# Optimization experiments

Measured on AMD Instinct MI355X. Metric: run time of the kernel, lower is better.

The kernel has to match this reference:

```python
import jax, jax.numpy as jnp
import numpy as np

T, B, I, H, L = 512, 64, 512, 1024, 2

def setup_inputs() -> dict:
    key = jax.random.key(0)
    ks = jax.random.split(key, 9)
    stdv = 1.0 / np.sqrt(H)
    u = lambda k, shape: jax.random.uniform(k, shape, jnp.float32, -stdv, stdv)
    return {
        "x": jax.random.normal(ks[0], (T, B, I), jnp.float32),
        "w_ih0": u(ks[1], (4 * H, I)),
        "w_hh0": u(ks[2], (4 * H, H)),
        "b_ih0": u(ks[3], (4 * H,)),
        "b_hh0": u(ks[4], (4 * H,)),
        "w_ih1": u(ks[5], (4 * H, H)),
        "w_hh1": u(ks[6], (4 * H, H)),
        "b_ih1": u(ks[7], (4 * H,)),
        "b_hh1": u(ks[8], (4 * H,)),
    }

def _lstm_cell(x, h, c, w_ih, w_hh, b_ih, b_hh):
    # gates: [B, 4H]
    gates = x @ w_ih.T + b_ih + h @ w_hh.T + b_hh
    i, f, g, o = jnp.split(gates, 4, axis=1)
    c_new = jax.nn.sigmoid(f) * c + jax.nn.sigmoid(i) * jnp.tanh(g)
    h_new = jax.nn.sigmoid(o) * jnp.tanh(c_new)
    return h_new, c_new

def reference(x, w_ih0, w_hh0, b_ih0, b_hh0, w_ih1, w_hh1, b_ih1, b_hh1):
    layers = [(w_ih0, w_hh0, b_ih0, b_hh0), (w_ih1, w_hh1, b_ih1, b_hh1)]
    h0 = jnp.zeros((L, B, H), x.dtype)
    c0 = jnp.zeros((L, B, H), x.dtype)

    def step(carry, x_t):
        h, c = carry
        inp = x_t
        hs, cs = [], []
        for l, (w_ih, w_hh, b_ih, b_hh) in enumerate(layers):
            h_new, c_new = _lstm_cell(inp, h[l], c[l], w_ih, w_hh, b_ih, b_hh)
            hs.append(h_new)
            cs.append(c_new)
            inp = h_new
        return (jnp.stack(hs), jnp.stack(cs)), inp

    (h_f, c_f), out = jax.lax.scan(step, (h0, c0), x)
    return out, (h_f, c_f)
```

## Files before the change

### kernel.cpp

```cpp
#include <hip/hip_runtime.h>

#define TT 512
#define BB 64
#define II 512
#define HH 1024
#define NBLK 256
#define NTHR 512
#define NCTR 32
#define CSTRIDE 32

typedef short bf16x8 __attribute__((ext_vector_type(8)));
typedef float f32x4 __attribute__((ext_vector_type(4)));
typedef int   i32x4 __attribute__((ext_vector_type(4)));

struct Params {
  const unsigned short* xb;
  unsigned short* h0;
  unsigned short* h1;
  unsigned int* ctr;
  const float* wih0; const float* whh0; const float* bih0; const float* bhh0;
  const float* wih1; const float* whh1; const float* bih1; const float* bhh1;
  float* out;
};

__device__ __forceinline__ unsigned short f2bf(float f) {
  unsigned int u = __float_as_uint(f);
  u += 0x7fffu + ((u >> 16) & 1u);
  return (unsigned short)(u >> 16);
}

__device__ __forceinline__ bf16x8 ld_bypass(const unsigned short* p) {
  i32x4 r;
  asm volatile("global_load_dwordx4 %0, %1, off sc0 sc1" : "=v"(r) : "v"(p));
  return __builtin_bit_cast(bf16x8, r);
}

__device__ __forceinline__ void st_bypass_u16(unsigned short* p, unsigned int v) {
  asm volatile("global_store_short %0, %1, off sc0 sc1" :: "v"(p), "v"(v) : "memory");
}

__global__ void cvt_kernel(const float* __restrict__ x, unsigned short* __restrict__ xb, int n8) {
  int i = blockIdx.x * blockDim.x + threadIdx.x;
  int stride = gridDim.x * blockDim.x;
  for (; i < n8; i += stride) {
    const float4* p = (const float4*)(x) + (size_t)i * 2;
    float4 a = p[0], b = p[1];
    bf16x8 v;
    v[0] = (short)f2bf(a.x); v[1] = (short)f2bf(a.y); v[2] = (short)f2bf(a.z); v[3] = (short)f2bf(a.w);
    v[4] = (short)f2bf(b.x); v[5] = (short)f2bf(b.y); v[6] = (short)f2bf(b.z); v[7] = (short)f2bf(b.w);
    ((bf16x8*)xb)[i] = v;
  }
}

__device__ __forceinline__ void gridbar(unsigned int* ctr, unsigned int target, int tid) {
  asm volatile("s_waitcnt vmcnt(0)" ::: "memory");
  __syncthreads();
  if (tid == 0)
    __hip_atomic_fetch_add(&ctr[(blockIdx.x & (NCTR - 1)) * CSTRIDE], 1u,
                           __ATOMIC_RELAXED, __HIP_MEMORY_SCOPE_AGENT);
  if (tid < NCTR) {
    while (__hip_atomic_load(&ctr[tid * CSTRIDE], __ATOMIC_RELAXED,
                             __HIP_MEMORY_SCOPE_AGENT) < target) {
      __builtin_amdgcn_s_sleep(1);
    }
  }
  __syncthreads();
}

template <int LAYER>
__device__ void body(const Params& P, float (*pbuf)[64][36], float (*cb)[16]) {
  constexpr int K   = (LAYER == 0) ? (II + HH) : (2 * HH);
  constexpr int KSL = K / (8 * 32);
  constexpr int KB  = KSL / 2;
  constexpr int KIH = (LAYER == 0) ? II : HH;

  const int tid  = threadIdx.x;
  const int lane = tid & 63;
  const int kh   = tid >> 6;
  const int lbid = blockIdx.x & 127;
  const int mh   = lbid >> 6;
  const int ns   = lbid & 63;
  const int l15  = lane & 15;
  const int lk8  = (lane >> 4) * 8;

  const float* wih = (LAYER == 0) ? P.wih0 : P.wih1;
  const float* whh = (LAYER == 0) ? P.whh0 : P.whh1;

  bf16x8 wf[4][KSL];
  #pragma unroll
  for (int nt = 0; nt < 4; ++nt) {
    const int row = nt * HH + ns * 16 + l15;
    #pragma unroll
    for (int ks = 0; ks < KSL; ++ks) {
      int k = kh * (KSL * 32) + ks * 32 + lk8;
      const float* src = (k < KIH) ? (wih + (size_t)row * KIH + k)
                                   : (whh + (size_t)row * HH + (k - KIH));
      const float4* p4 = (const float4*)src;
      float4 a = p4[0], b = p4[1];
      bf16x8 v;
      v[0] = (short)f2bf(a.x); v[1] = (short)f2bf(a.y); v[2] = (short)f2bf(a.z); v[3] = (short)f2bf(a.w);
      v[4] = (short)f2bf(b.x); v[5] = (short)f2bf(b.y); v[6] = (short)f2bf(b.z); v[7] = (short)f2bf(b.w);
      wf[nt][ks] = v;
    }
  }

  float bv[4];
  {
    const float* bi = (LAYER == 0) ? P.bih0 : P.bih1;
    const float* bh = (LAYER == 0) ? P.bhh0 : P.bhh1;
    int unit = ns * 16 + (tid & 15);
    #pragma unroll
    for (int g = 0; g < 4; ++g) bv[g] = bi[g * HH + unit] + bh[g * HH + unit];
  }

  if (tid < 128) {
    int q = tid >> 4, j = tid & 15;
    #pragma unroll
    for (int r = 0; r < 4; ++r) cb[q * 4 + r][j] = 0.f;
  }

  const size_t BH  = (size_t)BB * HH;
  const size_t TBH = (size_t)TT * BH;

  #pragma unroll 1
  for (int p = 0; p <= TT; ++p) {
    const int t = (LAYER == 0) ? p : p - 1;
    const bool active = (LAYER == 0) ? (p < TT) : (p >= 1);

    f32x4 acc[2][4];
    if (active) {
      #pragma unroll
      for (int mt = 0; mt < 2; ++mt)
        #pragma unroll
        for (int nt = 0; nt < 4; ++nt) acc[mt][nt] = f32x4{0.f, 0.f, 0.f, 0.f};

      const unsigned short* h0prev = P.h0 + (size_t)((t + 1) & 1) * BH;
      const unsigned short* h0cur  = P.h0 + (size_t)(t & 1) * BH;
      const unsigned short* h1prev = P.h1 + (size_t)((t + 1) & 1) * BH;

      #pragma unroll
      for (int half = 0; half < 2; ++half) {
        bf16x8 af[KB][2];
        #pragma unroll
        for (int ksb = 0; ksb < KB; ++ksb) {
          const int ks = half * KB + ksb;
          const int k  = kh * (KSL * 32) + ks * 32 + lk8;
          #pragma unroll
          for (int mt = 0; mt < 2; ++mt) {
            const int m = mh * 32 + mt * 16 + l15;
            if (LAYER == 0) {
              if (k < II) af[ksb][mt] = *(const bf16x8*)(P.xb + ((size_t)t * BB + m) * II + k);
              else        af[ksb][mt] = ld_bypass(h0prev + (size_t)m * HH + (k - II));
            } else {
              if (k < HH) af[ksb][mt] = ld_bypass(h0cur + (size_t)m * HH + k);
              else        af[ksb][mt] = ld_bypass(h1prev + (size_t)m * HH + (k - HH));
            }
          }
        }
        asm volatile("s_waitcnt vmcnt(0)" ::: "memory");
        __builtin_amdgcn_sched_barrier(0);
        #pragma unroll
        for (int ksb = 0; ksb < KB; ++ksb) {
          const int ks = half * KB + ksb;
          #pragma unroll
          for (int mt = 0; mt < 2; ++mt)
            #pragma unroll
            for (int nt = 0; nt < 4; ++nt)
              acc[mt][nt] = __builtin_amdgcn_mfma_f32_16x16x32_bf16(af[ksb][mt], wf[nt][ks], acc[mt][nt], 0, 0, 0);
        }
      }

      if (kh >= 4) {
        #pragma unroll
        for (int mt = 0; mt < 2; ++mt)
          #pragma unroll
          for (int nt = 0; nt < 4; ++nt) {
            int col = nt * 16 + l15;
            int mb  = mt * 16 + (lane >> 4) * 4;
            *(f32x4*)&pbuf[kh - 4][col][mb] = acc[mt][nt];
          }
      }
    }
    __syncthreads();
    if (active && kh < 4) {
      #pragma unroll
      for (int mt = 0; mt < 2; ++mt)
        #pragma unroll
        for (int nt = 0; nt < 4; ++nt) {
          int col = nt * 16 + l15;
          int mb  = mt * 16 + (lane >> 4) * 4;
          f32x4 v = *(const f32x4*)&pbuf[kh][col][mb];
          acc[mt][nt] += v;
          *(f32x4*)&pbuf[kh][col][mb] = acc[mt][nt];
        }
    }
    __syncthreads();
    if (active && tid < 128) {
      int q = tid >> 4, j = tid & 15;
      f32x4 gv[4];
      #pragma unroll
      for (int g = 0; g < 4; ++g) {
        int col = g * 16 + j;
        f32x4 s = *(const f32x4*)&pbuf[0][col][q * 4];
        #pragma unroll
        for (int w = 1; w < 4; ++w) s += *(const f32x4*)&pbuf[w][col][q * 4];
        gv[g] = s;
      }
      #pragma unroll
      for (int r = 0; r < 4; ++r) {
        int m = q * 4 + r;
        float iv = 1.f / (1.f + __expf(-(gv[0][r] + bv[0])));
        float fv = 1.f / (1.f + __expf(-(gv[1][r] + bv[1])));
        float gg = tanhf(gv[2][r] + bv[2]);
        float ov = 1.f / (1.f + __expf(-(gv[3][r] + bv[3])));
        float c = fv * cb[m][j] + iv * gg;
        cb[m][j] = c;
        float h = ov * tanhf(c);
        int mg = mh * 32 + m;
        int unit = ns * 16 + j;
        unsigned int hb = f2bf(h);
        if (LAYER == 0) {
          st_bypass_u16(P.h0 + (size_t)(t & 1) * BH + (size_t)mg * HH + unit, hb);
          if (t == TT - 1) P.out[TBH + (size_t)mg * HH + unit] = h;
        } else {
          st_bypass_u16(P.h1 + (size_t)(t & 1) * BH + (size_t)mg * HH + unit, hb);
          P.out[(size_t)t * BH + (size_t)mg * HH + unit] = h;
          if (t == TT - 1) P.out[TBH + BH + (size_t)mg * HH + unit] = h;
        }
      }
    }
    gridbar(P.ctr, (unsigned)(NBLK / NCTR) * (unsigned)(p + 1), tid);
  }

  if (tid < 128) {
    int q = tid >> 4, j = tid & 15;
    #pragma unroll
    for (int r = 0; r < 4; ++r) {
      int m = q * 4 + r;
      int mg = mh * 32 + m;
      int unit = ns * 16 + j;
      P.out[TBH + (size_t)(2 + LAYER) * BH + (size_t)mg * HH + unit] = cb[m][j];
    }
  }
}

__global__ void __launch_bounds__(NTHR, 2) lstm_kernel(Params P) {
  __shared__ float pbuf[4][64][36];
  __shared__ float cb[32][16];
  if (blockIdx.x < 128) body<0>(P, pbuf, cb);
  else                  body<1>(P, pbuf, cb);
}

extern "C" void kernel_launch(void* const* d_in, const int* in_sizes, int n_in,
                              void* d_out, int out_size, void* d_ws, size_t ws_size,
                              hipStream_t stream) {
  const float* x = (const float*)d_in[0];
  Params P;
  P.wih0 = (const float*)d_in[1];
  P.whh0 = (const float*)d_in[2];
  P.bih0 = (const float*)d_in[3];
  P.bhh0 = (const float*)d_in[4];
  P.wih1 = (const float*)d_in[5];
  P.whh1 = (const float*)d_in[6];
  P.bih1 = (const float*)d_in[7];
  P.bhh1 = (const float*)d_in[8];
  P.out  = (float*)d_out;

  char* ws = (char*)d_ws;
  P.ctr = (unsigned int*)ws;
  P.xb  = (const unsigned short*)(ws + 8192);
  unsigned short* xb_w = (unsigned short*)(ws + 8192);
  P.h0  = (unsigned short*)(ws + 8192 + (size_t)TT * BB * II * 2);
  P.h1  = P.h0 + (size_t)2 * BB * HH;

  hipMemsetAsync((void*)P.ctr, 0, 8192, stream);
  hipMemsetAsync((void*)P.h0, 0, (size_t)4 * BB * HH * sizeof(unsigned short), stream);

  int n8 = TT * BB * II / 8;
  cvt_kernel<<<2048, 256, 0, stream>>>(x, xb_w, n8);

  void* args[] = { &P };
  hipLaunchCooperativeKernel((void*)lstm_kernel, dim3(NBLK), dim3(NTHR), args, 0, stream);
}
```

Baseline: 4.356 ms.

## Stage h in LDS for vector stores, early barrier arrive, pipelined A-loads

Hidden-state outputs are first staged in shared memory, then written with 128-bit cache-bypassing stores instead of scattered 16-bit stores. The grid barrier is split so a block signals arrival right after its h stores, and the fp32 output writes happen before it waits. The A-fragment loads become a double-buffered pipeline in groups of two k-slices with partial vmcnt waits, and the launch-bounds occupancy hint drops from 2 to 1 block per CU, which frees registers. This targets per-step latency on the critical path of the recurrent chain, at the cost of an extra __syncthreads and added register pressure.

```diff
diff --git a/kernel.cpp b/kernel.cpp
--- a/kernel.cpp
+++ b/kernel.cpp
@@ -35,8 +35,8 @@
   return __builtin_bit_cast(bf16x8, r);
 }
 
-__device__ __forceinline__ void st_bypass_u16(unsigned short* p, unsigned int v) {
-  asm volatile("global_store_short %0, %1, off sc0 sc1" :: "v"(p), "v"(v) : "memory");
+__device__ __forceinline__ void st_bypass_b128(unsigned short* p, i32x4 v) {
+  asm volatile("global_store_dwordx4 %0, %1, off sc0 sc1" :: "v"(p), "v"(v) : "memory");
 }
 
 __global__ void cvt_kernel(const float* __restrict__ x, unsigned short* __restrict__ xb, int n8) {
@@ -52,26 +52,12 @@
   }
 }
 
-__device__ __forceinline__ void gridbar(unsigned int* ctr, unsigned int target, int tid) {
-  asm volatile("s_waitcnt vmcnt(0)" ::: "memory");
-  __syncthreads();
-  if (tid == 0)
-    __hip_atomic_fetch_add(&ctr[(blockIdx.x & (NCTR - 1)) * CSTRIDE], 1u,
-                           __ATOMIC_RELAXED, __HIP_MEMORY_SCOPE_AGENT);
-  if (tid < NCTR) {
-    while (__hip_atomic_load(&ctr[tid * CSTRIDE], __ATOMIC_RELAXED,
-                             __HIP_MEMORY_SCOPE_AGENT) < target) {
-      __builtin_amdgcn_s_sleep(1);
-    }
-  }
-  __syncthreads();
-}
-
 template <int LAYER>
-__device__ void body(const Params& P, float (*pbuf)[64][36], float (*cb)[16]) {
+__device__ void body(const Params& P, float (*pbuf)[64][36], float (*cb)[16],
+                     unsigned short (*hbuf)[16]) {
   constexpr int K   = (LAYER == 0) ? (II + HH) : (2 * HH);
   constexpr int KSL = K / (8 * 32);
-  constexpr int KB  = KSL / 2;
+  constexpr int NG  = KSL / 2;
   constexpr int KIH = (LAYER == 0) ? II : HH;
 
   const int tid  = threadIdx.x;
@@ -128,6 +114,7 @@
     const bool active = (LAYER == 0) ? (p < TT) : (p >= 1);
 
     f32x4 acc[2][4];
+    float hv[4];
     if (active) {
       #pragma unroll
       for (int mt = 0; mt < 2; ++mt)
@@ -138,36 +125,46 @@
       const unsigned short* h0cur  = P.h0 + (size_t)(t & 1) * BH;
       const unsigned short* h1prev = P.h1 + (size_t)((t + 1) & 1) * BH;
 
-      #pragma unroll
-      for (int half = 0; half < 2; ++half) {
-        bf16x8 af[KB][2];
-        #pragma unroll
-        for (int ksb = 0; ksb < KB; ++ksb) {
-          const int ks = half * KB + ksb;
+      bf16x8 af[2][2][2];
+
+      auto issue_group = [&](int g, int pp) {
+        #pragma unroll
+        for (int ksb = 0; ksb < 2; ++ksb) {
+          const int ks = g * 2 + ksb;
           const int k  = kh * (KSL * 32) + ks * 32 + lk8;
           #pragma unroll
           for (int mt = 0; mt < 2; ++mt) {
             const int m = mh * 32 + mt * 16 + l15;
+            const unsigned short* src;
             if (LAYER == 0) {
-              if (k < II) af[ksb][mt] = *(const bf16x8*)(P.xb + ((size_t)t * BB + m) * II + k);
-              else        af[ksb][mt] = ld_bypass(h0prev + (size_t)m * HH + (k - II));
+              src = (k < II) ? (P.xb + ((size_t)t * BB + m) * II + k)
+                             : (h0prev + (size_t)m * HH + (k - II));
             } else {
-              if (k < HH) af[ksb][mt] = ld_bypass(h0cur + (size_t)m * HH + k);
-              else        af[ksb][mt] = ld_bypass(h1prev + (size_t)m * HH + (k - HH));
+              src = (k < HH) ? (h0cur + (size_t)m * HH + k)
+                             : (h1prev + (size_t)m * HH + (k - HH));
             }
+            af[pp][ksb][mt] = ld_bypass(src);
           }
         }
-        asm volatile("s_waitcnt vmcnt(0)" ::: "memory");
+      };
+
+      issue_group(0, 0);
+      issue_group(1, 1);
+      #pragma unroll
+      for (int g = 0; g < NG; ++g) {
+        if (g < NG - 1) asm volatile("s_waitcnt vmcnt(4)" ::: "memory");
+        else            asm volatile("s_waitcnt vmcnt(0)" ::: "memory");
         __builtin_amdgcn_sched_barrier(0);
         #pragma unroll
-        for (int ksb = 0; ksb < KB; ++ksb) {
-          const int ks = half * KB + ksb;
+        for (int ksb = 0; ksb < 2; ++ksb) {
+          const int ks = g * 2 + ksb;
           #pragma unroll
           for (int mt = 0; mt < 2; ++mt)
             #pragma unroll
             for (int nt = 0; nt < 4; ++nt)
-              acc[mt][nt] = __builtin_amdgcn_mfma_f32_16x16x32_bf16(af[ksb][mt], wf[nt][ks], acc[mt][nt], 0, 0, 0);
+              acc[mt][nt] = __builtin_amdgcn_mfma_f32_16x16x32_bf16(af[g & 1][ksb][mt], wf[nt][ks], acc[mt][nt], 0, 0, 0);
         }
+        if (g + 2 < NG) issue_group(g + 2, g & 1);
       }
 
       if (kh >= 4) {
@@ -216,20 +213,47 @@
         float c = fv * cb[m][j] + iv * gg;
         cb[m][j] = c;
         float h = ov * tanhf(c);
-        int mg = mh * 32 + m;
+        hv[r] = h;
+        hbuf[m][j] = f2bf(h);
+      }
+    }
+    __syncthreads();
+    if (tid < 64) {
+      if (active) {
+        int row  = tid >> 1;
+        int half = tid & 1;
+        i32x4 v = *(const i32x4*)&hbuf[row][half * 8];
+        unsigned short* dst = ((LAYER == 0) ? P.h0 : P.h1) +
+            (size_t)(t & 1) * BH + (size_t)(mh * 32 + row) * HH + ns * 16 + half * 8;
+        st_bypass_b128(dst, v);
+      }
+      asm volatile("s_waitcnt vmcnt(0)" ::: "memory");
+      if (tid == 0)
+        __hip_atomic_fetch_add(&P.ctr[(blockIdx.x & (NCTR - 1)) * CSTRIDE], 1u,
+                               __ATOMIC_RELAXED, __HIP_MEMORY_SCOPE_AGENT);
+    }
+    if (active && tid < 128) {
+      int q = tid >> 4, j = tid & 15;
+      #pragma unroll
+      for (int r = 0; r < 4; ++r) {
+        int mg = mh * 32 + q * 4 + r;
         int unit = ns * 16 + j;
-        unsigned int hb = f2bf(h);
         if (LAYER == 0) {
-          st_bypass_u16(P.h0 + (size_t)(t & 1) * BH + (size_t)mg * HH + unit, hb);
-          if (t == TT - 1) P.out[TBH + (size_t)mg * HH + unit] = h;
+          if (t == TT - 1) P.out[TBH + (size_t)mg * HH + unit] = hv[r];
         } else {
-          st_bypass_u16(P.h1 + (size_t)(t & 1) * BH + (size_t)mg * HH + unit, hb);
-          P.out[(size_t)t * BH + (size_t)mg * HH + unit] = h;
-          if (t == TT - 1) P.out[TBH + BH + (size_t)mg * HH + unit] = h;
+          P.out[(size_t)t * BH + (size_t)mg * HH + unit] = hv[r];
+          if (t == TT - 1) P.out[TBH + BH + (size_t)mg * HH + unit] = hv[r];
         }
       }
     }
-    gridbar(P.ctr, (unsigned)(NBLK / NCTR) * (unsigned)(p + 1), tid);
+    if (tid < NCTR) {
+      unsigned int target = (unsigned)(NBLK / NCTR) * (unsigned)(p + 1);
+      while (__hip_atomic_load(&P.ctr[tid * CSTRIDE], __ATOMIC_RELAXED,
+                               __HIP_MEMORY_SCOPE_AGENT) < target) {
+        __builtin_amdgcn_s_sleep(1);
+      }
+    }
+    __syncthreads();
   }
 
   if (tid < 128) {
@@ -244,11 +268,12 @@
   }
 }
 
-__global__ void __launch_bounds__(NTHR, 2) lstm_kernel(Params P) {
+__global__ void __launch_bounds__(NTHR, 1) lstm_kernel(Params P) {
   __shared__ float pbuf[4][64][36];
   __shared__ float cb[32][16];
-  if (blockIdx.x < 128) body<0>(P, pbuf, cb);
-  else                  body<1>(P, pbuf, cb);
+  __shared__ unsigned short hbuf[32][16];
+  if (blockIdx.x < 128) body<0>(P, pbuf, cb, hbuf);
+  else                  body<1>(P, pbuf, cb, hbuf);
 }
 
 extern "C" void kernel_launch(void* const* d_in, const int* in_sizes, int n_in,
```

After: 4.456 ms. +2.3%, slower.
